# Kernel tuning notes

Measured on AMD Instinct MI355X. Metric: run time of the kernel, lower is better.

## Reference

```python
import jax, jax.numpy as jnp
import numpy as np
from jax.scipy.linalg import expm

B = 131072
ROT_DIM = 32   # rot_latent_dim
TRZ_DIM = 32   # tranz_latent_dim
W = 128        # MLP_hidden_layer_width


def setup_inputs() -> dict:
    key = jax.random.key(0)
    ks = jax.random.split(key, 13)
    def g(k, shape, scale):
        return jax.random.normal(k, shape, dtype=jnp.float32) * scale
    return {
        "y": g(ks[0], (B, ROT_DIM + TRZ_DIM), 1.0),
        # omega MLP: 32 -> 128 -> 128 -> 9
        "ow0": g(ks[1], (W, ROT_DIM), 1.0 / np.sqrt(ROT_DIM)),
        "ob0": g(ks[2], (W,), 0.01),
        "ow1": g(ks[3], (W, W), 1.0 / np.sqrt(W)),
        "ob1": g(ks[4], (W,), 0.01),
        "ow2": g(ks[5], (9, W), 1.0 / np.sqrt(W)),
        "ob2": g(ks[6], (9,), 0.01),
        # tranz MLP: 32 -> 128 -> 128 -> 3
        "tw0": g(ks[7], (W, TRZ_DIM), 1.0 / np.sqrt(TRZ_DIM)),
        "tb0": g(ks[8], (W,), 0.01),
        "tw1": g(ks[9], (W, W), 1.0 / np.sqrt(W)),
        "tb1": g(ks[10], (W,), 0.01),
        "tw2": g(ks[11], (3, W), 1.0 / np.sqrt(W)),
        "tb2": g(ks[12], (3,), 0.01),
    }


def _mlp(x, weights, biases):
    # eqx.nn.Linear: W @ x + b; ReLU on all but last layer
    n = len(weights)
    for i, (w, b) in enumerate(zip(weights, biases)):
        x = jnp.einsum("bi,oi->bo", x, w) + b
        if i + 1 < n:
            x = jax.nn.relu(x)
    return x


def reference(y, ow0, ob0, ow1, ob1, ow2, ob2, tw0, tb0, tw1, tb1, tw2, tb2):
    x = y[:, :ROT_DIM]            # dynamic_slice(0, rot_latent_dim)
    z = y[:, ROT_DIM:ROT_DIM + TRZ_DIM]
    omega = _mlp(x, [ow0, ow1, ow2], [ob0, ob1, ob2])       # [B, 9]
    # exp_omega: reshape to 3x3, matrix exponential, flatten back
    rot = jax.vmap(expm)(omega.reshape(B, 3, 3)).reshape(B, 9)
    trz = _mlp(z, [tw0, tw1, tw2], [tb0, tb1, tb2])          # [B, 3]
    return jnp.concatenate([rot, trz], axis=1)               # [B, 12]
```

## Files before the change

### kernel.cpp

```cpp
#include <hip/hip_runtime.h>
#include <hip/hip_bf16.h>
#include <stdint.h>

typedef short  short8  __attribute__((ext_vector_type(8)));
typedef float  floatx4 __attribute__((ext_vector_type(4)));

#define WS_W0_ROT   0
#define WS_W0_TRZ   8192
#define WS_W1_ROT   16384
#define WS_W1_TRZ   49152
#define WS_W2_ROT   81920
#define WS_W2_TRZ   86016
#define WS_BIAS     90112

__device__ __forceinline__ unsigned short f2bf_rne(float f) {
    union { float f; unsigned u; } v; v.f = f;
    unsigned r = v.u + 0x7fffu + ((v.u >> 16) & 1u);
    return (unsigned short)(r >> 16);
}

__global__ void prep_kernel(const float* __restrict__ ow0, const float* __restrict__ ow1,
                            const float* __restrict__ ow2, const float* __restrict__ tw0,
                            const float* __restrict__ tw1, const float* __restrict__ tw2,
                            const float* __restrict__ ob0, const float* __restrict__ ob1,
                            const float* __restrict__ ob2, const float* __restrict__ tb0,
                            const float* __restrict__ tb1, const float* __restrict__ tb2,
                            unsigned char* __restrict__ ws)
{
    int t = blockIdx.x * 256 + threadIdx.x;
    unsigned short* w16 = (unsigned short*)ws;
    if (t < 4096) {
        w16[t] = f2bf_rne(ow0[t]);
    } else if (t < 8192) {
        w16[t] = f2bf_rne(tw0[t - 4096]);
    } else if (t < 24576) {
        int i = t - 8192; int n = i >> 7, p = i & 127;
        w16[t] = f2bf_rne(ow1[n * 128 + ((p & 7) << 4) + (p >> 3)]);
    } else if (t < 40960) {
        int i = t - 24576; int n = i >> 7, p = i & 127;
        w16[t] = f2bf_rne(tw1[n * 128 + ((p & 7) << 4) + (p >> 3)]);
    } else if (t < 43008) {
        int i = t - 40960; int n = i >> 7, p = i & 127;
        w16[t] = (n < 9) ? f2bf_rne(ow2[n * 128 + ((p & 7) << 4) + (p >> 3)]) : (unsigned short)0;
    } else if (t < 45056) {
        int i = t - 43008; int n = i >> 7, p = i & 127;
        w16[t] = (n < 3) ? f2bf_rne(tw2[n * 128 + ((p & 7) << 4) + (p >> 3)]) : (unsigned short)0;
    } else if (t < 45600) {
        int i = t - 45056;
        float v;
        if      (i < 128) v = ob0[i];
        else if (i < 256) v = ob1[i - 128];
        else if (i < 272) v = (i - 256 < 9) ? ob2[i - 256] : 0.0f;
        else if (i < 400) v = tb0[i - 272];
        else if (i < 528) v = tb1[i - 400];
        else              v = (i - 528 < 3) ? tb2[i - 528] : 0.0f;
        ((float*)(ws + WS_BIAS))[i] = v;
    }
}

__device__ __forceinline__ floatx4 mfma16(short8 a, short8 b, floatx4 c) {
    return __builtin_amdgcn_mfma_f32_16x16x32_bf16(a, b, c, 0, 0, 0);
}

__device__ __forceinline__ short8 pack8(floatx4 a, floatx4 b) {
    union { unsigned u[4]; short8 s; } r;
    union { __hip_bfloat162 b2; unsigned u; } c;
    c.b2 = __float22bfloat162_rn(make_float2(a[0], a[1])); r.u[0] = c.u;
    c.b2 = __float22bfloat162_rn(make_float2(a[2], a[3])); r.u[1] = c.u;
    c.b2 = __float22bfloat162_rn(make_float2(b[0], b[1])); r.u[2] = c.u;
    c.b2 = __float22bfloat162_rn(make_float2(b[2], b[3])); r.u[3] = c.u;
    return r.s;
}

__device__ __forceinline__ void write_h_pair(char* hb, int q, int ln, int ntp,
                                             floatx4 aA, floatx4 aB) {
    #pragma unroll
    for (int r = 0; r < 4; ++r) {
        float lo = fmaxf(aA[r], 0.0f), hi = fmaxf(aB[r], 0.0f);
        union { __hip_bfloat162 b2; unsigned u; } c;
        c.b2 = __float22bfloat162_rn(make_float2(lo, hi));
        int m = q * 4 + r;
        int w = (ln * 4 + ntp) ^ ((m & 7) << 2);
        *(unsigned*)(hb + m * 256 + w * 4) = c.u;
    }
}

__device__ __forceinline__ void mat3mul(float* C, const float* A, const float* B) {
    #pragma unroll
    for (int i = 0; i < 3; ++i)
        #pragma unroll
        for (int j = 0; j < 3; ++j)
            C[i*3+j] = A[i*3+0]*B[0+j] + A[i*3+1]*B[3+j] + A[i*3+2]*B[6+j];
}

__launch_bounds__(256, 2)
__global__ void fused_main(const float* __restrict__ y,
                           const unsigned char* __restrict__ ws,
                           float* __restrict__ out)
{
    __shared__ __align__(16) unsigned char lds_h[4 * 4096];
    __shared__ float lds_stage[256 * 13];

    const int tid  = threadIdx.x;
    const int wv   = tid >> 6;
    const int lane = tid & 63;
    const int ln   = lane & 15;
    const int q    = lane >> 4;
    const int mlp  = wv >> 1;
    const int rh   = wv & 1;
    const int wgbase = blockIdx.x * 256;

    const int W0_OFF = mlp ? WS_W0_TRZ : WS_W0_ROT;
    const int W1_OFF = mlp ? WS_W1_TRZ : WS_W1_ROT;
    const int W2_OFF = mlp ? WS_W2_TRZ : WS_W2_ROT;
    const float* bias = (const float*)(ws + WS_BIAS) + (mlp ? 272 : 0);

    short8 bw0[8], bw1[32], bw2[4];
    #pragma unroll
    for (int nt = 0; nt < 8; ++nt)
        bw0[nt] = *(const short8*)(ws + W0_OFF + ((nt * 16 + ln) * 32 + q * 8) * 2);
    #pragma unroll
    for (int nt = 0; nt < 8; ++nt) {
        #pragma unroll
        for (int s2 = 0; s2 < 4; ++s2)
            bw1[nt * 4 + s2] = *(const short8*)(ws + W1_OFF + ((nt * 16 + ln) * 128 + s2 * 32 + q * 8) * 2);
    }
    #pragma unroll
    for (int s2 = 0; s2 < 4; ++s2)
        bw2[s2] = *(const short8*)(ws + W2_OFF + (ln * 128 + s2 * 32 + q * 8) * 2);

    float b0v[8], b1v[8];
    #pragma unroll
    for (int nt = 0; nt < 8; ++nt) {
        b0v[nt] = bias[nt * 16 + ln];
        b1v[nt] = bias[128 + nt * 16 + ln];
    }
    const float b2v = bias[256 + ln];

    char* hb = (char*)lds_h + wv * 4096;
    const int cb     = mlp ? 9 : 0;
    const int nvalid = mlp ? 3 : 9;

    #pragma unroll 1
    for (int g = 0; g < 8; ++g) {
        const int row0 = wgbase + rh * 128 + g * 16;

        const float* yp = y + (size_t)(row0 + ln) * 64 + mlp * 32 + q * 8;
        floatx4 y0 = *(const floatx4*)yp;
        floatx4 y1 = *(const floatx4*)(yp + 4);
        short8 a0 = pack8(y0, y1);

        #pragma unroll
        for (int ntp = 0; ntp < 4; ++ntp) {
            float bA = b0v[2*ntp], bB = b0v[2*ntp+1];
            floatx4 aA = {bA, bA, bA, bA};
            floatx4 aB = {bB, bB, bB, bB};
            aA = mfma16(a0, bw0[2*ntp],   aA);
            aB = mfma16(a0, bw0[2*ntp+1], aB);
            write_h_pair(hb, q, ln, ntp, aA, aB);
        }

        short8 a1[4];
        #pragma unroll
        for (int s2 = 0; s2 < 4; ++s2) {
            int w = (s2 * 16 + q * 4) ^ ((ln & 7) << 2);
            a1[s2] = *(const short8*)(hb + ln * 256 + w * 4);
        }

        #pragma unroll
        for (int ntp = 0; ntp < 4; ++ntp) {
            float bA = b1v[2*ntp], bB = b1v[2*ntp+1];
            floatx4 aA = {bA, bA, bA, bA};
            floatx4 aB = {bB, bB, bB, bB};
            #pragma unroll
            for (int s2 = 0; s2 < 4; ++s2) {
                aA = mfma16(a1[s2], bw1[(2*ntp)   * 4 + s2], aA);
                aB = mfma16(a1[s2], bw1[(2*ntp+1) * 4 + s2], aB);
            }
            write_h_pair(hb, q, ln, ntp, aA, aB);
        }

        short8 a2[4];
        #pragma unroll
        for (int s2 = 0; s2 < 4; ++s2) {
            int w = (s2 * 16 + q * 4) ^ ((ln & 7) << 2);
            a2[s2] = *(const short8*)(hb + ln * 256 + w * 4);
        }

        floatx4 acc = {b2v, b2v, b2v, b2v};
        #pragma unroll
        for (int s2 = 0; s2 < 4; ++s2)
            acc = mfma16(a2[s2], bw2[s2], acc);

        if (ln < nvalid) {
            const int rl = rh * 128 + g * 16 + q * 4;
            #pragma unroll
            for (int r = 0; r < 4; ++r)
                lds_stage[(rl + r) * 13 + cb + ln] = acc[r];
        }
    }

    __syncthreads();

    const int row_l = wv * 64 + lane;
    const float* st = &lds_stage[row_l * 13];
    float M[9], Rm[9];
    #pragma unroll
    for (int i = 0; i < 9; ++i) M[i] = st[i];
    const float tz0 = st[9], tz1 = st[10], tz2 = st[11];

    float r0 = fabsf(M[0]) + fabsf(M[1]) + fabsf(M[2]);
    float r1 = fabsf(M[3]) + fabsf(M[4]) + fabsf(M[5]);
    float r2 = fabsf(M[6]) + fabsf(M[7]) + fabsf(M[8]);
    float nrm = fmaxf(r0, fmaxf(r1, r2));
    int e; (void)frexpf(nrm, &e);
    int s = e + 1;
    if (s < 0) s = 0;
    if (s > 24) s = 24;
    float sc;
    { union { unsigned u; float f; } cv; cv.u = (unsigned)(127 - s) << 23; sc = cv.f; }
    #pragma unroll
    for (int i = 0; i < 9; ++i) M[i] *= sc;

    #pragma unroll
    for (int i = 0; i < 9; ++i) Rm[i] = 0.0f;
    Rm[0] = Rm[4] = Rm[8] = 1.0f;
    #pragma unroll
    for (int j = 12; j >= 1; --j) {
        float T[9]; mat3mul(T, M, Rm);
        const float inv = 1.0f / (float)j;
        #pragma unroll
        for (int i = 0; i < 9; ++i) Rm[i] = T[i] * inv;
        Rm[0] += 1.0f; Rm[4] += 1.0f; Rm[8] += 1.0f;
    }
    for (int it = 0; it < s; ++it) {
        float T[9]; mat3mul(T, Rm, Rm);
        #pragma unroll
        for (int i = 0; i < 9; ++i) Rm[i] = T[i];
    }

    float* op = out + (size_t)(wgbase + row_l) * 12;
    floatx4 o0 = {Rm[0], Rm[1], Rm[2], Rm[3]};
    floatx4 o1 = {Rm[4], Rm[5], Rm[6], Rm[7]};
    floatx4 o2 = {Rm[8], tz0, tz1, tz2};
    *(floatx4*)(op)     = o0;
    *(floatx4*)(op + 4) = o1;
    *(floatx4*)(op + 8) = o2;
}

extern "C" void kernel_launch(void* const* d_in, const int* in_sizes, int n_in,
                              void* d_out, int out_size, void* d_ws, size_t ws_size,
                              hipStream_t stream)
{
    const float* y = (const float*)d_in[0];
    prep_kernel<<<179, 256, 0, stream>>>(
        (const float*)d_in[1], (const float*)d_in[3], (const float*)d_in[5],
        (const float*)d_in[7], (const float*)d_in[9], (const float*)d_in[11],
        (const float*)d_in[2], (const float*)d_in[4], (const float*)d_in[6],
        (const float*)d_in[8], (const float*)d_in[10], (const float*)d_in[12],
        (unsigned char*)d_ws);
    fused_main<<<512, 256, 0, stream>>>(y, (const unsigned char*)d_ws, (float*)d_out);
}
```

Baseline: 145.4 us.

## Widen LDS hidden-layer accesses, prefetch next y tile, coalesce output stores via LDS

Hidden activations are now written to LDS as 128-bit rows with a new XOR swizzle instead of 32-bit scattered writes. The next group's y rows are prefetched one iteration ahead to hide global load latency. Layer 0 and layer 1 biases are packed into bf16 pairs to cut register use. The stage buffer is padded to 12 floats so each row can be read as vectors, and final outputs are staged back through LDS for fully coalesced stores. Storing biases in bf16 slightly changes numerics, and the added barrier and prefetch cost some overhead.

```diff
diff --git a/kernel.cpp b/kernel.cpp
--- a/kernel.cpp
+++ b/kernel.cpp
@@ -72,16 +72,30 @@
     return r.s;
 }
 
-__device__ __forceinline__ void write_h_pair(char* hb, int q, int ln, int ntp,
-                                             floatx4 aA, floatx4 aB) {
+__device__ __forceinline__ void write_h_b128(char* hb, int q, int ln,
+                                             const floatx4* acc) {
     #pragma unroll
     for (int r = 0; r < 4; ++r) {
-        float lo = fmaxf(aA[r], 0.0f), hi = fmaxf(aB[r], 0.0f);
-        union { __hip_bfloat162 b2; unsigned u; } c;
-        c.b2 = __float22bfloat162_rn(make_float2(lo, hi));
-        int m = q * 4 + r;
-        int w = (ln * 4 + ntp) ^ ((m & 7) << 2);
-        *(unsigned*)(hb + m * 256 + w * 4) = c.u;
+        const int m = q * 4 + r;
+        union { unsigned u[4]; short8 s; } pk;
+        #pragma unroll
+        for (int j = 0; j < 4; ++j) {
+            float lo = fmaxf(acc[2 * j][r], 0.0f);
+            float hi = fmaxf(acc[2 * j + 1][r], 0.0f);
+            union { __hip_bfloat162 b2; unsigned u; } c;
+            c.b2 = __float22bfloat162_rn(make_float2(lo, hi));
+            pk.u[j] = c.u;
+        }
+        const int cp = ln ^ (m & 15);
+        *(short8*)(hb + m * 256 + cp * 16) = pk.s;
+    }
+}
+
+__device__ __forceinline__ void read_a_b128(const char* hb, int q, int ln, short8* a) {
+    #pragma unroll
+    for (int s2 = 0; s2 < 4; ++s2) {
+        const int cp = (s2 * 4 + q) ^ (ln & 15);
+        a[s2] = *(const short8*)(hb + ln * 256 + cp * 16);
     }
 }
 
@@ -98,8 +112,8 @@
                            const unsigned char* __restrict__ ws,
                            float* __restrict__ out)
 {
-    __shared__ __align__(16) unsigned char lds_h[4 * 4096];
-    __shared__ float lds_stage[256 * 13];
+    __shared__ __align__(16) unsigned char lds_h[4][4096];
+    __shared__ __align__(16) float lds_stage[256 * 12];
 
     const int tid  = threadIdx.x;
     const int wv   = tid >> 6;
@@ -129,123 +143,135 @@
     for (int s2 = 0; s2 < 4; ++s2)
         bw2[s2] = *(const short8*)(ws + W2_OFF + (ln * 128 + s2 * 32 + q * 8) * 2);
 
-    float b0v[8], b1v[8];
+    unsigned b01[8];
     #pragma unroll
     for (int nt = 0; nt < 8; ++nt) {
-        b0v[nt] = bias[nt * 16 + ln];
-        b1v[nt] = bias[128 + nt * 16 + ln];
+        union { __hip_bfloat162 b2; unsigned u; } c;
+        c.b2 = __float22bfloat162_rn(make_float2(bias[nt * 16 + ln], bias[128 + nt * 16 + ln]));
+        b01[nt] = c.u;
     }
     const float b2v = bias[256 + ln];
 
-    char* hb = (char*)lds_h + wv * 4096;
+    char* hb = (char*)lds_h[wv];
     const int cb     = mlp ? 9 : 0;
     const int nvalid = mlp ? 3 : 9;
 
+    const float* ybase = y + (size_t)(wgbase + rh * 128) * 64 + mlp * 32 + q * 8;
+
+    floatx4 cy0 = *(const floatx4*)(ybase + (size_t)ln * 64);
+    floatx4 cy1 = *(const floatx4*)(ybase + (size_t)ln * 64 + 4);
+    short8 a0 = pack8(cy0, cy1);
+
     #pragma unroll 1
     for (int g = 0; g < 8; ++g) {
-        const int row0 = wgbase + rh * 128 + g * 16;
-
-        const float* yp = y + (size_t)(row0 + ln) * 64 + mlp * 32 + q * 8;
-        floatx4 y0 = *(const floatx4*)yp;
-        floatx4 y1 = *(const floatx4*)(yp + 4);
-        short8 a0 = pack8(y0, y1);
-
-        #pragma unroll
-        for (int ntp = 0; ntp < 4; ++ntp) {
-            float bA = b0v[2*ntp], bB = b0v[2*ntp+1];
-            floatx4 aA = {bA, bA, bA, bA};
-            floatx4 aB = {bB, bB, bB, bB};
-            aA = mfma16(a0, bw0[2*ntp],   aA);
-            aB = mfma16(a0, bw0[2*ntp+1], aB);
-            write_h_pair(hb, q, ln, ntp, aA, aB);
-        }
+        const int gn = (g < 7) ? g + 1 : g;
+        const float* yp = ybase + (size_t)(gn * 16 + ln) * 64;
+        floatx4 ny0 = *(const floatx4*)yp;
+        floatx4 ny1 = *(const floatx4*)(yp + 4);
+
+        floatx4 acc[8];
+        #pragma unroll
+        for (int nt = 0; nt < 8; ++nt) {
+            union { __hip_bfloat162 b2; unsigned u; } c; c.u = b01[nt];
+            float b = __bfloat162float(c.b2.x);
+            floatx4 a = {b, b, b, b};
+            acc[nt] = mfma16(a0, bw0[nt], a);
+        }
+        write_h_b128(hb, q, ln, acc);
+
+        a0 = pack8(ny0, ny1);
 
         short8 a1[4];
-        #pragma unroll
-        for (int s2 = 0; s2 < 4; ++s2) {
-            int w = (s2 * 16 + q * 4) ^ ((ln & 7) << 2);
-            a1[s2] = *(const short8*)(hb + ln * 256 + w * 4);
-        }
-
-        #pragma unroll
-        for (int ntp = 0; ntp < 4; ++ntp) {
-            float bA = b1v[2*ntp], bB = b1v[2*ntp+1];
-            floatx4 aA = {bA, bA, bA, bA};
-            floatx4 aB = {bB, bB, bB, bB};
-            #pragma unroll
-            for (int s2 = 0; s2 < 4; ++s2) {
-                aA = mfma16(a1[s2], bw1[(2*ntp)   * 4 + s2], aA);
-                aB = mfma16(a1[s2], bw1[(2*ntp+1) * 4 + s2], aB);
-            }
-            write_h_pair(hb, q, ln, ntp, aA, aB);
-        }
+        read_a_b128(hb, q, ln, a1);
+
+        #pragma unroll
+        for (int nt = 0; nt < 8; ++nt) {
+            union { __hip_bfloat162 b2; unsigned u; } c; c.u = b01[nt];
+            float b = __bfloat162float(c.b2.y);
+            floatx4 a = {b, b, b, b};
+            #pragma unroll
+            for (int s2 = 0; s2 < 4; ++s2)
+                a = mfma16(a1[s2], bw1[nt * 4 + s2], a);
+            acc[nt] = a;
+        }
+        write_h_b128(hb, q, ln, acc);
 
         short8 a2[4];
-        #pragma unroll
-        for (int s2 = 0; s2 < 4; ++s2) {
-            int w = (s2 * 16 + q * 4) ^ ((ln & 7) << 2);
-            a2[s2] = *(const short8*)(hb + ln * 256 + w * 4);
-        }
-
-        floatx4 acc = {b2v, b2v, b2v, b2v};
+        read_a_b128(hb, q, ln, a2);
+
+        floatx4 acc2 = {b2v, b2v, b2v, b2v};
         #pragma unroll
         for (int s2 = 0; s2 < 4; ++s2)
-            acc = mfma16(a2[s2], bw2[s2], acc);
+            acc2 = mfma16(a2[s2], bw2[s2], acc2);
 
         if (ln < nvalid) {
             const int rl = rh * 128 + g * 16 + q * 4;
             #pragma unroll
             for (int r = 0; r < 4; ++r)
-                lds_stage[(rl + r) * 13 + cb + ln] = acc[r];
+                lds_stage[(rl + r) * 12 + cb + ln] = acc2[r];
         }
     }
 
     __syncthreads();
 
-    const int row_l = wv * 64 + lane;
-    const float* st = &lds_stage[row_l * 13];
-    float M[9], Rm[9];
-    #pragma unroll
-    for (int i = 0; i < 9; ++i) M[i] = st[i];
-    const float tz0 = st[9], tz1 = st[10], tz2 = st[11];
-
-    float r0 = fabsf(M[0]) + fabsf(M[1]) + fabsf(M[2]);
-    float r1 = fabsf(M[3]) + fabsf(M[4]) + fabsf(M[5]);
-    float r2 = fabsf(M[6]) + fabsf(M[7]) + fabsf(M[8]);
-    float nrm = fmaxf(r0, fmaxf(r1, r2));
-    int e; (void)frexpf(nrm, &e);
-    int s = e + 1;
-    if (s < 0) s = 0;
-    if (s > 24) s = 24;
-    float sc;
-    { union { unsigned u; float f; } cv; cv.u = (unsigned)(127 - s) << 23; sc = cv.f; }
-    #pragma unroll
-    for (int i = 0; i < 9; ++i) M[i] *= sc;
-
-    #pragma unroll
-    for (int i = 0; i < 9; ++i) Rm[i] = 0.0f;
-    Rm[0] = Rm[4] = Rm[8] = 1.0f;
-    #pragma unroll
-    for (int j = 12; j >= 1; --j) {
-        float T[9]; mat3mul(T, M, Rm);
-        const float inv = 1.0f / (float)j;
-        #pragma unroll
-        for (int i = 0; i < 9; ++i) Rm[i] = T[i] * inv;
-        Rm[0] += 1.0f; Rm[4] += 1.0f; Rm[8] += 1.0f;
-    }
-    for (int it = 0; it < s; ++it) {
-        float T[9]; mat3mul(T, Rm, Rm);
-        #pragma unroll
-        for (int i = 0; i < 9; ++i) Rm[i] = T[i];
-    }
-
-    float* op = out + (size_t)(wgbase + row_l) * 12;
-    floatx4 o0 = {Rm[0], Rm[1], Rm[2], Rm[3]};
-    floatx4 o1 = {Rm[4], Rm[5], Rm[6], Rm[7]};
-    floatx4 o2 = {Rm[8], tz0, tz1, tz2};
-    *(floatx4*)(op)     = o0;
-    *(floatx4*)(op + 4) = o1;
-    *(floatx4*)(op + 8) = o2;
+    {
+        float* st = &lds_stage[tid * 12];
+        floatx4 m0 = *(floatx4*)(st);
+        floatx4 m1 = *(floatx4*)(st + 4);
+        floatx4 m2 = *(floatx4*)(st + 8);
+        float M[9] = {m0[0], m0[1], m0[2], m0[3], m1[0], m1[1], m1[2], m1[3], m2[0]};
+        const float tz0 = m2[1], tz1 = m2[2], tz2 = m2[3];
+
+        float r0 = fabsf(M[0]) + fabsf(M[1]) + fabsf(M[2]);
+        float r1 = fabsf(M[3]) + fabsf(M[4]) + fabsf(M[5]);
+        float r2 = fabsf(M[6]) + fabsf(M[7]) + fabsf(M[8]);
+        float nrm = fmaxf(r0, fmaxf(r1, r2));
+        int e; (void)frexpf(nrm, &e);
+        int s = e + 1;
+        if (s < 0) s = 0;
+        if (s > 24) s = 24;
+        float sc;
+        { union { unsigned u; float f; } cv; cv.u = (unsigned)(127 - s) << 23; sc = cv.f; }
+        #pragma unroll
+        for (int i = 0; i < 9; ++i) M[i] *= sc;
+
+        float Rm[9];
+        #pragma unroll
+        for (int i = 0; i < 9; ++i) Rm[i] = 0.0f;
+        Rm[0] = Rm[4] = Rm[8] = 1.0f;
+        #pragma unroll
+        for (int j = 12; j >= 1; --j) {
+            float T[9]; mat3mul(T, M, Rm);
+            const float inv = 1.0f / (float)j;
+            #pragma unroll
+            for (int i = 0; i < 9; ++i) Rm[i] = T[i] * inv;
+            Rm[0] += 1.0f; Rm[4] += 1.0f; Rm[8] += 1.0f;
+        }
+        for (int it = 0; it < s; ++it) {
+            float T[9]; mat3mul(T, Rm, Rm);
+            #pragma unroll
+            for (int i = 0; i < 9; ++i) Rm[i] = T[i];
+        }
+
+        floatx4 o0 = {Rm[0], Rm[1], Rm[2], Rm[3]};
+        floatx4 o1 = {Rm[4], Rm[5], Rm[6], Rm[7]};
+        floatx4 o2 = {Rm[8], tz0, tz1, tz2};
+        *(floatx4*)(st)     = o0;
+        *(floatx4*)(st + 4) = o1;
+        *(floatx4*)(st + 8) = o2;
+    }
+
+    __syncthreads();
+
+    {
+        float* ob = out + (size_t)wgbase * 12;
+        #pragma unroll
+        for (int k = 0; k < 3; ++k) {
+            const int j = k * 256 + tid;
+            floatx4 v = *(floatx4*)&lds_stage[j * 4];
+            *(floatx4*)(ob + j * 4) = v;
+        }
+    }
 }
 
 extern "C" void kernel_launch(void* const* d_in, const int* in_sizes, int n_in,
```

New measurement: 143.7 us. No clear change (-1.2%).
